# Kernel optimization log

Measured on AMD Instinct MI355X. Metric: run time of the kernel, lower is better.

Reference implementation:

```python
import jax, jax.numpy as jnp
import numpy as np

B, S, D, V, ND = 8, 512, 1024, 32000, 8


def setup_inputs() -> dict:
    key = jax.random.key(0)
    k1, k2, k3, k4 = jax.random.split(key, 4)
    scale = 0.02
    return {
        "hidden_states": jax.random.normal(k1, (B, S, D), dtype=jnp.float32),
        "domain_ids": jax.random.randint(k2, (B,), 0, ND + 1),  # index ND triggers default head
        "W_base": jax.random.normal(k3, (D, D), dtype=jnp.float32) * scale,
        "b_base": jnp.zeros((D,), dtype=jnp.float32),
        # slots 0..ND-1 are domain heads, slot ND is the default head
        "W_heads": jax.random.normal(k4, (ND + 1, D, V), dtype=jnp.float32) * scale,
        "b_heads": jnp.zeros((ND + 1, V), dtype=jnp.float32),
    }


def reference(hidden_states, domain_ids, W_base, b_base, W_heads, b_heads):
    # base_projection: Linear(D, D)
    hidden = jnp.einsum("bsd,de->bse", hidden_states, W_base) + b_base
    num_domains = W_heads.shape[0] - 1
    # out-of-range domain ids fall back to the default head (last slot)
    idx = jnp.where((domain_ids >= 0) & (domain_ids < num_domains), domain_ids, num_domains)
    Wg = W_heads[idx]              # [B, D, V] gathered per-example head weights
    bg = b_heads[idx]              # [B, V]
    out = jnp.einsum("bsd,bdv->bsv", hidden, Wg) + bg[:, None, :]
    return out
```

## Files before the change

### kernel.cpp

```cpp
#include <hip/hip_runtime.h>
#include <hip/hip_bf16.h>


#define BCNT 8
#define SLEN 512
#define DDIM 1024
#define VDIM 32000
#define NDOM 8

typedef __attribute__((ext_vector_type(4))) float f32x4;
typedef __attribute__((ext_vector_type(8))) short bf16x8;

static __device__ __forceinline__ unsigned short f2bf(float f) {
    union { float f; unsigned int u; } x; x.f = f;
    unsigned int u = x.u;
    return (unsigned short)((u + 0x7FFFu + ((u >> 16) & 1u)) >> 16);
}

static __device__ __forceinline__ unsigned int pack2(float lo, float hi) {
    return (unsigned int)f2bf(lo) | ((unsigned int)f2bf(hi) << 16);
}

#define SBAR()   __builtin_amdgcn_s_barrier()
#define SCHED0() __builtin_amdgcn_sched_barrier(0)

__global__ __launch_bounds__(256)
void gemm1_k(const float* __restrict__ Af, const float* __restrict__ Bbase,
             const float* __restrict__ bias, __hip_bfloat16* __restrict__ Cb,
             int Mrows)
{
    __shared__ __align__(16) __hip_bfloat16 lds_a[128 * 64];
    __shared__ __align__(16) unsigned int   lds_b[32 * 128];

    const int tid  = threadIdx.x;
    const int lane = tid & 63;
    const int w    = tid >> 6;

    const int nwg = gridDim.x;
    const int bid = blockIdx.x;
    const int q   = nwg >> 3;
    const int sid = (bid & 7) * q + (bid >> 3);

    const int MT = Mrows >> 7;
    const int mt = sid % MT;
    const int nt = sid / MT;
    const int m0 = mt << 7;
    const int n0 = nt << 7;

    f32x4 acc[4][4];
    #pragma unroll
    for (int m = 0; m < 4; ++m)
        #pragma unroll
        for (int n = 0; n < 4; ++n)
            acc[m][n] = (f32x4)0.0f;

    const int wr = w >> 1, wc = w & 1;
    const int lr = lane & 15, lg = lane >> 4;

    for (int kt = 0; kt < DDIM / 64; ++kt) {
        const int kbase = kt * 64;

        #pragma unroll
        for (int t = 0; t < 8; ++t) {
            const int flat = (t * 256 + tid) * 4;
            const int row = flat >> 6, col = flat & 63;
            const float4 v = *(const float4*)(Af + (size_t)(m0 + row) * DDIM + kbase + col);
            uint2 pp;
            pp.x = pack2(v.x, v.y);
            pp.y = pack2(v.z, v.w);
            *(uint2*)(lds_a + flat) = pp;
        }

        #pragma unroll
        for (int t = 0; t < 4; ++t) {
            const int id = t * 256 + tid;
            const int kk = id >> 5;
            const int n  = (id & 31) << 2;
            const float* b0 = Bbase + (size_t)(kbase + 2 * kk) * DDIM + n0 + n;
            const float4 e = *(const float4*)b0;
            const float4 o = *(const float4*)(b0 + DDIM);
            uint4 pw;
            pw.x = pack2(e.x, o.x);
            pw.y = pack2(e.y, o.y);
            pw.z = pack2(e.z, o.z);
            pw.w = pack2(e.w, o.w);
            const int ns = n ^ ((kk & 4) << 2);
            *(uint4*)&lds_b[kk * 128 + ns] = pw;
        }

        __syncthreads();

        #pragma unroll
        for (int ks = 0; ks < 2; ++ks) {
            bf16x8 af[4], bfr[4];
            #pragma unroll
            for (int m = 0; m < 4; ++m) {
                const int row = wr * 64 + m * 16 + lr;
                const int k   = ks * 32 + lg * 8;
                af[m] = *(const bf16x8*)&lds_a[row * 64 + k];
            }
            #pragma unroll
            for (int n = 0; n < 4; ++n) {
                const int col = wc * 64 + n * 16 + lr;
                const int kkb = ks * 16 + lg * 4;
                union { unsigned int u[4]; bf16x8 v; } cvt;
                #pragma unroll
                for (int j = 0; j < 4; ++j) {
                    const int kk = kkb + j;
                    const int ns = col ^ ((kk & 4) << 2);
                    cvt.u[j] = lds_b[kk * 128 + ns];
                }
                bfr[n] = cvt.v;
            }
            #pragma unroll
            for (int m = 0; m < 4; ++m)
                #pragma unroll
                for (int n = 0; n < 4; ++n)
                    acc[m][n] = __builtin_amdgcn_mfma_f32_16x16x32_bf16(af[m], bfr[n], acc[m][n], 0, 0, 0);
        }

        __syncthreads();
    }

    #pragma unroll
    for (int m = 0; m < 4; ++m) {
        #pragma unroll
        for (int n = 0; n < 4; ++n) {
            const int col = n0 + wc * 64 + n * 16 + lr;
            const float bv = bias[col];
            #pragma unroll
            for (int r = 0; r < 4; ++r) {
                const int row = m0 + wr * 64 + m * 16 + lg * 4 + r;
                Cb[(size_t)row * DDIM + col] = __hip_bfloat16_raw{f2bf(acc[m][n][r] + bv)};
            }
        }
    }
}

__global__ __launch_bounds__(512)
void gemm2_k(const __hip_bfloat16* __restrict__ A, const float* __restrict__ Wh,
             const float* __restrict__ bh, float* __restrict__ out,
             const int* __restrict__ dom)
{
    extern __shared__ __align__(16) char smem[];
    __hip_bfloat16* ldsA0 = (__hip_bfloat16*)smem;
    __hip_bfloat16* ldsA1 = (__hip_bfloat16*)(smem + 32768);
    unsigned int*   ldsB0 = (unsigned int*)(smem + 65536);
    unsigned int*   ldsB1 = (unsigned int*)(smem + 65536 + 16384);

    const int tid  = threadIdx.x;
    const int lane = tid & 63;
    const int w    = tid >> 6;
    const int wr   = w >> 1;
    const int wc   = w & 1;
    const int lr   = lane & 15;
    const int lg   = lane >> 4;

    const int bid = blockIdx.x;
    const int q   = gridDim.x >> 3;
    const int sid = (bid & 7) * q + (bid >> 3);
    const int mt   = sid & 1;
    const int rest = sid >> 1;
    const int nt   = rest % 250;
    const int ex   = rest / 250;
    const int m0   = ex * SLEN + mt * 256;
    const int n0   = nt * 128;

    const int di  = dom[ex];
    const int hid = (di >= 0 && di < NDOM) ? di : NDOM;
    const float* Bp   = Wh + (size_t)hid * DDIM * (size_t)VDIM;
    const float* bias = bh + (size_t)hid * (size_t)VDIM;

    f32x4 acc[4][4];
    #pragma unroll
    for (int m = 0; m < 4; ++m)
        #pragma unroll
        for (int n = 0; n < 4; ++n)
            acc[m][n] = (f32x4)0.0f;

    const int nb   = (tid & 63) * 2;
    const int kb   = (tid >> 6) * 8;
    const int bswz = (lane & 7) << 2;
    const int bslot = ((kb >> 1) ^ bswz);

    float2 br[8];

    #define LOADB(KT) do {                                                        \
        const float* _p = Bp + (size_t)((KT) * 64 + kb) * VDIM + n0 + nb;         \
        _Pragma("unroll")                                                         \
        for (int j = 0; j < 8; ++j) br[j] = *(const float2*)(_p + (size_t)j * VDIM); \
    } while (0)

    #define WRITEB(LB) do {                                                       \
        uint4 w0, w1;                                                             \
        w0.x = pack2(br[0].x, br[1].x); w0.y = pack2(br[2].x, br[3].x);           \
        w0.z = pack2(br[4].x, br[5].x); w0.w = pack2(br[6].x, br[7].x);           \
        w1.x = pack2(br[0].y, br[1].y); w1.y = pack2(br[2].y, br[3].y);           \
        w1.z = pack2(br[4].y, br[5].y); w1.w = pack2(br[6].y, br[7].y);           \
        *(uint4*)&(LB)[nb * 32 + bslot]       = w0;                               \
        *(uint4*)&(LB)[(nb + 1) * 32 + bslot] = w1;                               \
    } while (0)

    #define STAGEA(LA, KT) do {                                                   \
        _Pragma("unroll")                                                         \
        for (int i = 0; i < 4; ++i) {                                             \
            const int base_e = (i * 8 + w) * 512;                                 \
            const int flat   = base_e + lane * 8;                                 \
            const int row    = flat >> 6;                                         \
            const int kbyte  = (flat & 63) * 2;                                   \
            const int srck   = (kbyte ^ ((row & 7) << 4)) >> 1;                   \
            const __hip_bfloat16* src = A + (size_t)(m0 + row) * DDIM + (KT) * 64 + srck; \
            __builtin_amdgcn_global_load_lds(                                     \
                (const __attribute__((address_space(1))) unsigned int*)src,       \
                (__attribute__((address_space(3))) unsigned int*)((LA) + base_e), \
                16, 0, 0);                                                        \
        }                                                                         \
    } while (0)

    #define COMPUTE(LA, LB) do {                                                  \
        _Pragma("unroll")                                                         \
        for (int ks = 0; ks < 2; ++ks) {                                          \
            bf16x8 af[4], bfr[4];                                                 \
            _Pragma("unroll")                                                     \
            for (int m = 0; m < 4; ++m) {                                         \
                const int row = wr * 64 + m * 16 + lr;                            \
                const int kby = ks * 64 + lg * 16;                                \
                const int eff = kby ^ ((row & 7) << 4);                           \
                af[m] = *(const bf16x8*)&(LA)[row * 64 + (eff >> 1)];             \
            }                                                                     \
            _Pragma("unroll")                                                     \
            for (int n = 0; n < 4; ++n) {                                         \
                const int col  = wc * 64 + n * 16 + lr;                           \
                const int kkb  = ks * 16 + lg * 4;                                \
                const int slot = kkb ^ (((col >> 1) & 7) << 2);                   \
                bfr[n] = *(const bf16x8*)&(LB)[col * 32 + slot];                  \
            }                                                                     \
            _Pragma("unroll")                                                     \
            for (int m = 0; m < 4; ++m)                                           \
                _Pragma("unroll")                                                 \
                for (int n = 0; n < 4; ++n)                                       \
                    acc[m][n] = __builtin_amdgcn_mfma_f32_16x16x32_bf16(af[m], bfr[n], acc[m][n], 0, 0, 0); \
        }                                                                         \
    } while (0)

    LOADB(0);
    STAGEA(ldsA0, 0);
    SCHED0();
    WRITEB(ldsB0);
    LOADB(1);
    SCHED0();
    asm volatile("s_waitcnt vmcnt(8) lgkmcnt(0)" ::: "memory");
    SCHED0();
    SBAR();

    for (int kt = 0; kt < 16; ++kt) {
        __hip_bfloat16* la = (kt & 1) ? ldsA1 : ldsA0;
        __hip_bfloat16* ln = (kt & 1) ? ldsA0 : ldsA1;
        unsigned int*   lb = (kt & 1) ? ldsB1 : ldsB0;
        unsigned int*   lnb = (kt & 1) ? ldsB0 : ldsB1;

        if (kt < 15) {
            STAGEA(ln, kt + 1);
            SCHED0();
            WRITEB(lnb);
            if (kt < 14) LOADB(kt + 2);
            SCHED0();
        }

        COMPUTE(la, lb);

        if (kt < 15) {
            SCHED0();
            if (kt < 14) asm volatile("s_waitcnt vmcnt(8) lgkmcnt(0)" ::: "memory");
            else         asm volatile("s_waitcnt vmcnt(0) lgkmcnt(0)" ::: "memory");
            SCHED0();
            SBAR();
        }
    }

    #pragma unroll
    for (int n = 0; n < 4; ++n) {
        const int col = n0 + wc * 64 + n * 16 + lr;
        const float bv = bias[col];
        #pragma unroll
        for (int m = 0; m < 4; ++m) {
            #pragma unroll
            for (int r = 0; r < 4; ++r) {
                const int row = m0 + wr * 64 + m * 16 + lg * 4 + r;
                out[(size_t)row * VDIM + col] = acc[m][n][r] + bv;
            }
        }
    }

    #undef LOADB
    #undef WRITEB
    #undef STAGEA
    #undef COMPUTE
}

extern "C" void kernel_launch(void* const* d_in, const int* in_sizes, int n_in,
                              void* d_out, int out_size, void* d_ws, size_t ws_size,
                              hipStream_t stream)
{
    const float* hs  = (const float*)d_in[0];
    const int*   dom = (const int*)d_in[1];
    const float* Wb  = (const float*)d_in[2];
    const float* bb  = (const float*)d_in[3];
    const float* Wh  = (const float*)d_in[4];
    const float* bh  = (const float*)d_in[5];
    float* out = (float*)d_out;
    __hip_bfloat16* hidden = (__hip_bfloat16*)d_ws;

    const int M = BCNT * SLEN;

    const int g1 = (M / 128) * (DDIM / 128);
    hipLaunchKernelGGL(gemm1_k, dim3(g1), dim3(256), 0, stream, hs, Wb, bb, hidden, M);

    const int smem_bytes = 98304;
    static int attr_set = 0;
    if (!attr_set) {
        hipFuncSetAttribute((const void*)gemm2_k, hipFuncAttributeMaxDynamicSharedMemorySize, smem_bytes);
        attr_set = 1;
    }
    const int g2 = BCNT * (SLEN / 256) * (VDIM / 128);
    hipLaunchKernelGGL(gemm2_k, dim3(g2), dim3(512), smem_bytes, stream, hidden, Wh, bh, out, dom);
}
```

Measured before the change: 658.4 us.

## Shrink gemm2 to 128x128 single-buffered tiles for multiple blocks per CU

The second GEMM moves from 256x128 tiles with 512 threads and 96KB of double-buffered dynamic LDS to 128x128 tiles with 256 threads and about 32KB of single-buffered static LDS. Launch bounds now ask for 3 blocks per CU, so occupancy should carry the latency hiding instead of explicit double buffering. B loads become 16-byte float4 loads, and bf16 packing uses the hardware conversion intrinsic. In exchange, each W_heads tile is now read from global memory by twice as many M tiles, and barriers are added around the LDS refill.

```diff
diff --git a/kernel.cpp b/kernel.cpp
--- a/kernel.cpp
+++ b/kernel.cpp
@@ -18,7 +18,10 @@
 }
 
 static __device__ __forceinline__ unsigned int pack2(float lo, float hi) {
-    return (unsigned int)f2bf(lo) | ((unsigned int)f2bf(hi) << 16);
+    float2 t; t.x = lo; t.y = hi;
+    union { __hip_bfloat162 h; unsigned int u; } c;
+    c.h = __float22bfloat162_rn(t);
+    return c.u;
 }
 
 #define SBAR()   __builtin_amdgcn_s_barrier()
@@ -137,16 +140,13 @@
     }
 }
 
-__global__ __launch_bounds__(512)
+__global__ __launch_bounds__(256, 3)
 void gemm2_k(const __hip_bfloat16* __restrict__ A, const float* __restrict__ Wh,
              const float* __restrict__ bh, float* __restrict__ out,
              const int* __restrict__ dom)
 {
-    extern __shared__ __align__(16) char smem[];
-    __hip_bfloat16* ldsA0 = (__hip_bfloat16*)smem;
-    __hip_bfloat16* ldsA1 = (__hip_bfloat16*)(smem + 32768);
-    unsigned int*   ldsB0 = (unsigned int*)(smem + 65536);
-    unsigned int*   ldsB1 = (unsigned int*)(smem + 65536 + 16384);
+    __shared__ __align__(16) __hip_bfloat16 ldsA[128 * 64];
+    __shared__ __align__(16) unsigned int   ldsB[128 * 32];
 
     const int tid  = threadIdx.x;
     const int lane = tid & 63;
@@ -156,14 +156,14 @@
     const int lr   = lane & 15;
     const int lg   = lane >> 4;
 
-    const int bid = blockIdx.x;
-    const int q   = gridDim.x >> 3;
-    const int sid = (bid & 7) * q + (bid >> 3);
-    const int mt   = sid & 1;
-    const int rest = sid >> 1;
+    const int bid  = blockIdx.x;
+    const int q    = gridDim.x >> 3;
+    const int sid  = (bid & 7) * q + (bid >> 3);
+    const int mt   = sid & 3;
+    const int rest = sid >> 2;
     const int nt   = rest % 250;
     const int ex   = rest / 250;
-    const int m0   = ex * SLEN + mt * 256;
+    const int m0   = ex * SLEN + mt * 128;
     const int n0   = nt * 128;
 
     const int di  = dom[ex];
@@ -178,75 +178,80 @@
         for (int n = 0; n < 4; ++n)
             acc[m][n] = (f32x4)0.0f;
 
-    const int nb   = (tid & 63) * 2;
-    const int kb   = (tid >> 6) * 8;
-    const int bswz = (lane & 7) << 2;
-    const int bslot = ((kb >> 1) ^ bswz);
-
-    float2 br[8];
-
-    #define LOADB(KT) do {                                                        \
-        const float* _p = Bp + (size_t)((KT) * 64 + kb) * VDIM + n0 + nb;         \
-        _Pragma("unroll")                                                         \
-        for (int j = 0; j < 8; ++j) br[j] = *(const float2*)(_p + (size_t)j * VDIM); \
+    const int nb4 = (tid & 31) << 2;
+    const int kb  = (tid >> 5) << 3;
+    const int qb  = kb >> 1;
+
+    f32x4 br4[8];
+
+    #define LOADB(KT) do {                                                         \
+        const float* _p = Bp + (size_t)((KT) * 64 + kb) * VDIM + n0 + nb4;         \
+        _Pragma("unroll")                                                          \
+        for (int j = 0; j < 8; ++j) br4[j] = *(const f32x4*)(_p + (size_t)j * VDIM); \
     } while (0)
 
-    #define WRITEB(LB) do {                                                       \
-        uint4 w0, w1;                                                             \
-        w0.x = pack2(br[0].x, br[1].x); w0.y = pack2(br[2].x, br[3].x);           \
-        w0.z = pack2(br[4].x, br[5].x); w0.w = pack2(br[6].x, br[7].x);           \
-        w1.x = pack2(br[0].y, br[1].y); w1.y = pack2(br[2].y, br[3].y);           \
-        w1.z = pack2(br[4].y, br[5].y); w1.w = pack2(br[6].y, br[7].y);           \
-        *(uint4*)&(LB)[nb * 32 + bslot]       = w0;                               \
-        *(uint4*)&(LB)[(nb + 1) * 32 + bslot] = w1;                               \
+    #define WRITEB() do {                                                          \
+        _Pragma("unroll")                                                          \
+        for (int i = 0; i < 4; ++i) {                                              \
+            const int col  = nb4 + i;                                              \
+            const int slot = qb ^ (((col >> 1) & 7) << 2);                         \
+            uint4 wv;                                                              \
+            wv.x = pack2(br4[0][i], br4[1][i]);                                    \
+            wv.y = pack2(br4[2][i], br4[3][i]);                                    \
+            wv.z = pack2(br4[4][i], br4[5][i]);                                    \
+            wv.w = pack2(br4[6][i], br4[7][i]);                                    \
+            *(uint4*)&ldsB[col * 32 + slot] = wv;                                  \
+        }                                                                          \
     } while (0)
 
-    #define STAGEA(LA, KT) do {                                                   \
-        _Pragma("unroll")                                                         \
-        for (int i = 0; i < 4; ++i) {                                             \
-            const int base_e = (i * 8 + w) * 512;                                 \
-            const int flat   = base_e + lane * 8;                                 \
-            const int row    = flat >> 6;                                         \
-            const int kbyte  = (flat & 63) * 2;                                   \
-            const int srck   = (kbyte ^ ((row & 7) << 4)) >> 1;                   \
+    #define STAGEA(KT) do {                                                        \
+        _Pragma("unroll")                                                          \
+        for (int i = 0; i < 4; ++i) {                                              \
+            const int base_e = (i * 4 + w) * 512;                                  \
+            const int flat   = base_e + lane * 8;                                  \
+            const int row    = flat >> 6;                                          \
+            const int kbyte  = (flat & 63) * 2;                                    \
+            const int srck   = (kbyte ^ ((row & 7) << 4)) >> 1;                    \
             const __hip_bfloat16* src = A + (size_t)(m0 + row) * DDIM + (KT) * 64 + srck; \
-            __builtin_amdgcn_global_load_lds(                                     \
-                (const __attribute__((address_space(1))) unsigned int*)src,       \
-                (__attribute__((address_space(3))) unsigned int*)((LA) + base_e), \
-                16, 0, 0);                                                        \
-        }                                                                         \
+            __builtin_amdgcn_global_load_lds(                                      \
+                (const __attribute__((address_space(1))) unsigned int*)src,        \
+                (__attribute__((address_space(3))) unsigned int*)(ldsA + base_e),  \
+                16, 0, 0);                                                         \
+        }                                                                          \
     } while (0)
 
-    #define COMPUTE(LA, LB) do {                                                  \
-        _Pragma("unroll")                                                         \
-        for (int ks = 0; ks < 2; ++ks) {                                          \
-            bf16x8 af[4], bfr[4];                                                 \
-            _Pragma("unroll")                                                     \
-            for (int m = 0; m < 4; ++m) {                                         \
-                const int row = wr * 64 + m * 16 + lr;                            \
-                const int kby = ks * 64 + lg * 16;                                \
-                const int eff = kby ^ ((row & 7) << 4);                           \
-                af[m] = *(const bf16x8*)&(LA)[row * 64 + (eff >> 1)];             \
-            }                                                                     \
-            _Pragma("unroll")                                                     \
-            for (int n = 0; n < 4; ++n) {                                         \
-                const int col  = wc * 64 + n * 16 + lr;                           \
-                const int kkb  = ks * 16 + lg * 4;                                \
-                const int slot = kkb ^ (((col >> 1) & 7) << 2);                   \
-                bfr[n] = *(const bf16x8*)&(LB)[col * 32 + slot];                  \
-            }                                                                     \
-            _Pragma("unroll")                                                     \
-            for (int m = 0; m < 4; ++m)                                           \
-                _Pragma("unroll")                                                 \
-                for (int n = 0; n < 4; ++n)                                       \
+    #define COMPUTE() do {                                                         \
+        _Pragma("unroll")                                                          \
+        for (int ks = 0; ks < 2; ++ks) {                                           \
+            bf16x8 af[4], bfr[4];                                                  \
+            _Pragma("unroll")                                                      \
+            for (int m = 0; m < 4; ++m) {                                          \
+                const int row = wr * 64 + m * 16 + lr;                             \
+                const int kby = ks * 64 + lg * 16;                                 \
+                const int eff = kby ^ ((row & 7) << 4);                            \
+                af[m] = *(const bf16x8*)&ldsA[row * 64 + (eff >> 1)];              \
+            }                                                                      \
+            _Pragma("unroll")                                                      \
+            for (int n = 0; n < 4; ++n) {                                          \
+                const int col  = wc * 64 + n * 16 + lr;                            \
+                const int kkb  = ks * 16 + lg * 4;                                 \
+                const int slot = kkb ^ (((col >> 1) & 7) << 2);                    \
+                bfr[n] = *(const bf16x8*)&ldsB[col * 32 + slot];                   \
+            }                                                                      \
+            _Pragma("unroll")                                                      \
+            for (int m = 0; m < 4; ++m)                                            \
+                _Pragma("unroll")                                                  \
+                for (int n = 0; n < 4; ++n)                                        \
                     acc[m][n] = __builtin_amdgcn_mfma_f32_16x16x32_bf16(af[m], bfr[n], acc[m][n], 0, 0, 0); \
-        }                                                                         \
+        }                                                                          \
     } while (0)
 
     LOADB(0);
-    STAGEA(ldsA0, 0);
-    SCHED0();
-    WRITEB(ldsB0);
+    SCHED0();
+    STAGEA(0);
+    SCHED0();
+    WRITEB();
+    SCHED0();
     LOADB(1);
     SCHED0();
     asm volatile("s_waitcnt vmcnt(8) lgkmcnt(0)" ::: "memory");
@@ -254,25 +259,22 @@
     SBAR();
 
     for (int kt = 0; kt < 16; ++kt) {
-        __hip_bfloat16* la = (kt & 1) ? ldsA1 : ldsA0;
-        __hip_bfloat16* ln = (kt & 1) ? ldsA0 : ldsA1;
-        unsigned int*   lb = (kt & 1) ? ldsB1 : ldsB0;
-        unsigned int*   lnb = (kt & 1) ? ldsB0 : ldsB1;
-
+        COMPUTE();
         if (kt < 15) {
-            STAGEA(ln, kt + 1);
-            SCHED0();
-            WRITEB(lnb);
-            if (kt < 14) LOADB(kt + 2);
-            SCHED0();
-        }
-
-        COMPUTE(la, lb);
-
-        if (kt < 15) {
-            SCHED0();
-            if (kt < 14) asm volatile("s_waitcnt vmcnt(8) lgkmcnt(0)" ::: "memory");
-            else         asm volatile("s_waitcnt vmcnt(0) lgkmcnt(0)" ::: "memory");
+            SCHED0();
+            SBAR();
+            SCHED0();
+            STAGEA(kt + 1);
+            SCHED0();
+            WRITEB();
+            SCHED0();
+            if (kt < 14) {
+                LOADB(kt + 2);
+                SCHED0();
+                asm volatile("s_waitcnt vmcnt(8) lgkmcnt(0)" ::: "memory");
+            } else {
+                asm volatile("s_waitcnt vmcnt(0) lgkmcnt(0)" ::: "memory");
+            }
             SCHED0();
             SBAR();
         }
@@ -316,12 +318,6 @@
     const int g1 = (M / 128) * (DDIM / 128);
     hipLaunchKernelGGL(gemm1_k, dim3(g1), dim3(256), 0, stream, hs, Wb, bb, hidden, M);
 
-    const int smem_bytes = 98304;
-    static int attr_set = 0;
-    if (!attr_set) {
-        hipFuncSetAttribute((const void*)gemm2_k, hipFuncAttributeMaxDynamicSharedMemorySize, smem_bytes);
-        attr_set = 1;
-    }
-    const int g2 = BCNT * (SLEN / 256) * (VDIM / 128);
-    hipLaunchKernelGGL(gemm2_k, dim3(g2), dim3(512), smem_bytes, stream, hidden, Wh, bh, out, dom);
-}
+    const int g2 = BCNT * (SLEN / 128) * (VDIM / 128);
+    hipLaunchKernelGGL(gemm2_k, dim3(g2), dim3(256), 0, stream, hidden, Wh, bh, out, dom);
+}
```

Result: faster. 538.7 us (-18.2%).
